# Performance work log

Measured on AMD Instinct MI355X. Metric: run time of the kernel, lower is better.

Reference implementation:

```python
import jax, jax.numpy as jnp
import numpy as np

B, S, D, H, NE, M = 4, 512, 768, 12, 42, 8
OFFSET = 1  # bert cls offset


def setup_inputs() -> dict:
    key = jax.random.key(0)
    k1, k2, k3, k4 = jax.random.split(key, 4)
    sequence_output = jax.random.normal(k1, (B, S, D), dtype=jnp.float32)
    attention = jax.random.uniform(k2, (B, H, S, S), dtype=jnp.float32)
    mention_pos = jax.random.randint(k3, (B, NE, M), 0, S - 2, dtype=jnp.int32)
    mention_mask = jax.random.randint(k4, (B, NE, M), 0, 2, dtype=jnp.int32)
    mention_mask = mention_mask.at[..., 0].set(1)  # every entity has >=1 mention
    return {"sequence_output": sequence_output, "attention": attention,
            "mention_pos": mention_pos, "mention_mask": mention_mask}


def reference(sequence_output, attention, mention_pos, mention_mask):
    b, s, d = sequence_output.shape
    h = attention.shape[1]
    pos = mention_pos + OFFSET                      # [B,NE,M]
    valid = (mention_mask > 0) & (pos < s)          # start+offset < c check
    pos_c = jnp.clip(pos, 0, s - 1)
    bidx = jnp.arange(b)[:, None, None]

    # ragged gather of mention hidden states / attention rows
    emb_m = sequence_output[bidx, pos_c]            # [B,NE,M,D]
    att_m = attention[bidx, :, pos_c]               # [B,NE,M,H,S]

    # logsumexp pool over valid mentions (zeros if no valid mention)
    masked = jnp.where(valid[..., None], emb_m, -jnp.inf)
    lse = jax.scipy.special.logsumexp(masked, axis=2)          # [B,NE,D]
    has = valid.any(axis=2)
    ent_emb = jnp.where(has[..., None], lse, 0.0)

    # mean pool attention rows over valid mentions
    cnt = jnp.maximum(valid.sum(axis=2), 1).astype(att_m.dtype)
    ent_att = (att_m * valid[..., None, None].astype(att_m.dtype)).sum(axis=2) \
              / cnt[..., None, None]                            # [B,NE,H,S]

    # all-pairs head/tail entity embeddings (index_select over hts pairs)
    hs = jnp.broadcast_to(ent_emb[:, :, None, :], (b, NE, NE, d))
    ts = jnp.broadcast_to(ent_emb[:, None, :, :], (b, NE, NE, d))

    # context-based channel map: pairwise attention fusion
    ht = (ent_att[:, :, None] * ent_att[:, None, :]).mean(axis=3)  # [B,NE,NE,S]
    ht = ht / (ht.sum(axis=-1, keepdims=True) + 1e-5)
    rs = jnp.einsum('bsd,bijs->bijd', sequence_output, ht)         # [B,NE,NE,D]

    return jnp.concatenate([hs, ts, rs], axis=-1)  # [B,NE,NE,3D]
```

## Files before the change

kernel.cpp:

```cpp
#include <hip/hip_runtime.h>
#include <hip/hip_bf16.h>
#include <cfloat>
#include <cmath>

#define B_ 4
#define S_ 512
#define D_ 768
#define H_ 12
#define NE_ 42
#define M_ 8
#define OFFSET_ 1
#define NE2_ (NE_*NE_)
#define OUTC_ (3*D_)
#define HS_ (H_*S_)
#define MPAD_ 1792

typedef __attribute__((ext_vector_type(8))) short short8;
typedef __attribute__((ext_vector_type(4))) float f32x4;

#define GLOAD_LDS16(g, l) __builtin_amdgcn_global_load_lds( \
    (const __attribute__((address_space(1))) unsigned int*)(g), \
    (__attribute__((address_space(3))) unsigned int*)(l), 16, 0, 0)

__global__ void k_prep(const float* __restrict__ seq, __hip_bfloat16* __restrict__ seqT) {
    const int b  = blockIdx.z;
    const int s0 = blockIdx.y * 64;
    const int d0 = blockIdx.x * 64;
    const int t  = threadIdx.x;

    __shared__ float tile[64][65];
#pragma unroll
    for (int i = 0; i < 16; ++i) {
        const int r = (t >> 6) * 16 + i;
        const int c = t & 63;
        tile[r][c] = seq[((size_t)b * S_ + s0 + r) * D_ + d0 + c];
    }
    __syncthreads();
#pragma unroll
    for (int i = 0; i < 16; ++i) {
        const int r = (t >> 6) * 16 + i;
        const int c = t & 63;
        seqT[((size_t)b * D_ + d0 + r) * S_ + s0 + c] = __float2bfloat16(tile[c][r]);
    }
}

__global__ void k_ent_att(const float* __restrict__ att, const int* __restrict__ mpos,
                          const int* __restrict__ mmask, float* __restrict__ ent_att) {
    const int beh = blockIdx.x;
    const int h   = beh % H_;
    const int be  = beh / H_;
    const int b   = be / NE_;

    __shared__ int sp[M_];
    __shared__ int sv[M_];
    if (threadIdx.x < M_) {
        int p  = mpos[be * M_ + threadIdx.x] + OFFSET_;
        int v  = (mmask[be * M_ + threadIdx.x] > 0) && (p < S_);
        int pc = p < 0 ? 0 : (p > S_ - 1 ? S_ - 1 : p);
        sp[threadIdx.x] = pc;
        sv[threadIdx.x] = v;
    }
    __syncthreads();

    int cnt = 0;
#pragma unroll
    for (int m = 0; m < M_; ++m) cnt += sv[m];
    const float inv_cnt = 1.0f / (float)(cnt > 0 ? cnt : 1);

    const float* arow = att + ((size_t)b * H_ + h) * S_ * S_;
    const int s0 = threadIdx.x;
    const int s1 = threadIdx.x + 256;
    float a0 = 0.0f, a1 = 0.0f;
#pragma unroll
    for (int m = 0; m < M_; ++m) {
        if (sv[m]) {
            a0 += arow[(size_t)sp[m] * S_ + s0];
            a1 += arow[(size_t)sp[m] * S_ + s1];
        }
    }
    float* dst = ent_att + ((size_t)be * H_ + h) * S_;
    dst[s0] = a0 * inv_cnt;
    dst[s1] = a1 * inv_cnt;
}

__global__ void k_ent_emb(const float* __restrict__ seq, const int* __restrict__ mpos,
                          const int* __restrict__ mmask, float* __restrict__ ent_emb) {
    const int be = blockIdx.x;
    const int b  = be / NE_;

    __shared__ int sp[M_];
    __shared__ int sv[M_];
    if (threadIdx.x < M_) {
        int p  = mpos[be * M_ + threadIdx.x] + OFFSET_;
        int v  = (mmask[be * M_ + threadIdx.x] > 0) && (p < S_);
        int pc = p < 0 ? 0 : (p > S_ - 1 ? S_ - 1 : p);
        sp[threadIdx.x] = pc;
        sv[threadIdx.x] = v;
    }
    __syncthreads();

    int cnt = 0;
#pragma unroll
    for (int m = 0; m < M_; ++m) cnt += sv[m];
    const bool has = cnt > 0;

    for (int d = threadIdx.x; d < D_; d += blockDim.x) {
        float vals[M_];
        float mx = -FLT_MAX;
#pragma unroll
        for (int m = 0; m < M_; ++m) {
            float v = sv[m] ? seq[((size_t)b * S_ + sp[m]) * D_ + d] : -FLT_MAX;
            vals[m] = v;
            mx = fmaxf(mx, v);
        }
        float o = 0.0f;
        if (has) {
            float ss = 0.0f;
#pragma unroll
            for (int m = 0; m < M_; ++m)
                if (sv[m]) ss += expf(vals[m] - mx);
            o = mx + logf(ss);
        }
        ent_emb[(size_t)be * D_ + d] = o;
    }
}

__global__ void k_ht(const float* __restrict__ ent_att, __hip_bfloat16* __restrict__ htb) {
    const int ij = blockIdx.x;
    const int b  = blockIdx.y;
    const int s0 = threadIdx.x;
    const int s1 = threadIdx.x + 256;
    __hip_bfloat16* dst = htb + ((size_t)b * MPAD_ + ij) * S_;

    if (ij >= NE2_) {
        dst[s0] = __float2bfloat16(0.0f);
        dst[s1] = __float2bfloat16(0.0f);
        return;
    }
    const int i = ij / NE_;
    const int j = ij - i * NE_;

    const float* Ai = ent_att + ((size_t)b * NE_ + i) * HS_;
    const float* Aj = ent_att + ((size_t)b * NE_ + j) * HS_;

    float v0 = 0.0f, v1 = 0.0f;
#pragma unroll
    for (int h = 0; h < H_; ++h) {
        v0 += Ai[h * S_ + s0] * Aj[h * S_ + s0];
        v1 += Ai[h * S_ + s1] * Aj[h * S_ + s1];
    }
    v0 *= (1.0f / H_);
    v1 *= (1.0f / H_);

    float local = v0 + v1;
#pragma unroll
    for (int off = 32; off > 0; off >>= 1) local += __shfl_xor(local, off, 64);
    __shared__ float wsum[4];
    if ((threadIdx.x & 63) == 0) wsum[threadIdx.x >> 6] = local;
    __syncthreads();
    const float inv = 1.0f / (wsum[0] + wsum[1] + wsum[2] + wsum[3] + 1e-5f);

    dst[s0] = __float2bfloat16(v0 * inv);
    dst[s1] = __float2bfloat16(v1 * inv);
}

__global__ void __launch_bounds__(256)
k_gemm(const __hip_bfloat16* __restrict__ htb, const __hip_bfloat16* __restrict__ seqT,
       float* __restrict__ out) {
    const int b     = blockIdx.z;
    const int tileN = blockIdx.x * 128;
    const int tileM = blockIdx.y * 128;
    const int tid   = threadIdx.x;
    const int w     = tid >> 6;
    const int lane  = tid & 63;
    const int wr    = w >> 1;
    const int wc    = w & 1;

    __shared__ unsigned short As[128 * 32];
    __shared__ unsigned short Bs[128 * 32];

    const __hip_bfloat16* A = htb  + (size_t)b * MPAD_ * S_;
    const __hip_bfloat16* Bt = seqT + (size_t)b * D_ * S_;

    const int crow = lane >> 2;
    const int ccol = (lane & 3) * 8;

    const int lr = lane & 15;
    const int lk = (lane >> 4) * 8;

    f32x4 acc[4][4];
#pragma unroll
    for (int mf = 0; mf < 4; ++mf)
#pragma unroll
        for (int nf = 0; nf < 4; ++nf) acc[mf][nf] = (f32x4){0.f, 0.f, 0.f, 0.f};

    for (int k0 = 0; k0 < S_; k0 += 32) {
#pragma unroll
        for (int q = 0; q < 2; ++q) {
            const int c = w * 2 + q;
            const __hip_bfloat16* ga = A + (size_t)(tileM + c * 16 + crow) * S_ + k0 + ccol;
            GLOAD_LDS16(ga, As + c * 512);
            const __hip_bfloat16* gb = Bt + (size_t)(tileN + c * 16 + crow) * S_ + k0 + ccol;
            GLOAD_LDS16(gb, Bs + c * 512);
        }
        __syncthreads();

        short8 af[4], bf[4];
#pragma unroll
        for (int mf = 0; mf < 4; ++mf)
            af[mf] = *(const short8*)&As[(wr * 64 + mf * 16 + lr) * 32 + lk];
#pragma unroll
        for (int nf = 0; nf < 4; ++nf)
            bf[nf] = *(const short8*)&Bs[(wc * 64 + nf * 16 + lr) * 32 + lk];
#pragma unroll
        for (int mf = 0; mf < 4; ++mf)
#pragma unroll
            for (int nf = 0; nf < 4; ++nf)
                acc[mf][nf] = __builtin_amdgcn_mfma_f32_16x16x32_bf16(af[mf], bf[nf], acc[mf][nf], 0, 0, 0);
        __syncthreads();
    }

#pragma unroll
    for (int mf = 0; mf < 4; ++mf) {
        const int row0 = tileM + wr * 64 + mf * 16 + (lane >> 4) * 4;
#pragma unroll
        for (int nf = 0; nf < 4; ++nf) {
            const int col = tileN + wc * 64 + nf * 16 + (lane & 15);
#pragma unroll
            for (int j = 0; j < 4; ++j) {
                const int r = row0 + j;
                if (r < NE2_)
                    out[((size_t)(b * NE2_ + r)) * OUTC_ + 2 * D_ + col] = acc[mf][nf][j];
            }
        }
    }
}

__global__ void k_hsts(const float* __restrict__ ent_emb, float* __restrict__ out) {
    const int bij = blockIdx.x;
    const int b   = bij / NE2_;
    const int ij  = bij - b * NE2_;
    const int i   = ij / NE_;
    const int j   = ij - i * NE_;

    const float4* ei = reinterpret_cast<const float4*>(ent_emb + ((size_t)b * NE_ + i) * D_);
    const float4* ej = reinterpret_cast<const float4*>(ent_emb + ((size_t)b * NE_ + j) * D_);
    float4* o = reinterpret_cast<float4*>(out + (size_t)bij * OUTC_);

    for (int t = threadIdx.x; t < D_ / 4; t += blockDim.x) o[t] = ei[t];
    for (int t = threadIdx.x; t < D_ / 4; t += blockDim.x) o[D_ / 4 + t] = ej[t];
}

extern "C" void kernel_launch(void* const* d_in, const int* in_sizes, int n_in,
                              void* d_out, int out_size, void* d_ws, size_t ws_size,
                              hipStream_t stream) {
    const float* seq   = (const float*)d_in[0];
    const float* att   = (const float*)d_in[1];
    const int*   mpos  = (const int*)d_in[2];
    const int*   mmask = (const int*)d_in[3];
    float* out = (float*)d_out;

    float* ent_emb = (float*)d_ws;
    float* ent_att = ent_emb + (size_t)B_ * NE_ * D_;
    __hip_bfloat16* htb  = (__hip_bfloat16*)(ent_att + (size_t)B_ * NE_ * HS_);
    __hip_bfloat16* seqT = htb + (size_t)B_ * MPAD_ * S_;

    k_prep<<<dim3(D_ / 64, S_ / 64, B_), 256, 0, stream>>>(seq, seqT);
    k_ent_att<<<B_ * NE_ * H_, 256, 0, stream>>>(att, mpos, mmask, ent_att);
    k_ent_emb<<<B_ * NE_, 256, 0, stream>>>(seq, mpos, mmask, ent_emb);
    k_ht<<<dim3(MPAD_, B_), 256, 0, stream>>>(ent_att, htb);
    k_gemm<<<dim3(D_ / 128, MPAD_ / 128, B_), 256, 0, stream>>>(htb, seqT, out);
    k_hsts<<<B_ * NE2_, 256, 0, stream>>>(ent_emb, out);
}
```

Baseline: 149.9 us.

## Register-tile pairwise attention products and fold normalization into GEMM epilogue

Replaces the per-pair ht kernel with a kernel that stages an 8-column slice of every entity's attention in LDS. Each thread computes a 3x3 block of entity pairs, so each attention value is reused across many pairs instead of being re-read from global memory for every pair. The row-sum normalization is deferred: per-pair partial sums are accumulated into a zero-initialized buffer with atomics, and the GEMM epilogue scales each output row by the reciprocal, with the 1/H factor folded into the epsilon. This cuts redundant L2 traffic, at the cost of global atomics, an extra scalar load per output element in the epilogue, and padding rows of the A matrix that are no longer zeroed.

```diff
diff --git a/kernel.cpp b/kernel.cpp
--- a/kernel.cpp
+++ b/kernel.cpp
@@ -45,7 +45,16 @@
 }
 
 __global__ void k_ent_att(const float* __restrict__ att, const int* __restrict__ mpos,
-                          const int* __restrict__ mmask, float* __restrict__ ent_att) {
+                          const int* __restrict__ mmask, float* __restrict__ ent_att,
+                          float* __restrict__ Gsum) {
+    if (blockIdx.x < 7) {
+#pragma unroll
+        for (int k = 0; k < 4; ++k) {
+            const int idx = blockIdx.x * 1024 + k * 256 + threadIdx.x;
+            if (idx < B_ * NE2_) Gsum[idx] = 0.0f;
+        }
+    }
+
     const int beh = blockIdx.x;
     const int h   = beh % H_;
     const int be  = beh / H_;
@@ -125,48 +134,87 @@
     }
 }
 
-__global__ void k_ht(const float* __restrict__ ent_att, __hip_bfloat16* __restrict__ htb) {
-    const int ij = blockIdx.x;
-    const int b  = blockIdx.y;
-    const int s0 = threadIdx.x;
-    const int s1 = threadIdx.x + 256;
-    __hip_bfloat16* dst = htb + ((size_t)b * MPAD_ + ij) * S_;
-
-    if (ij >= NE2_) {
-        dst[s0] = __float2bfloat16(0.0f);
-        dst[s1] = __float2bfloat16(0.0f);
-        return;
-    }
-    const int i = ij / NE_;
-    const int j = ij - i * NE_;
-
-    const float* Ai = ent_att + ((size_t)b * NE_ + i) * HS_;
-    const float* Aj = ent_att + ((size_t)b * NE_ + j) * HS_;
-
-    float v0 = 0.0f, v1 = 0.0f;
-#pragma unroll
-    for (int h = 0; h < H_; ++h) {
-        v0 += Ai[h * S_ + s0] * Aj[h * S_ + s0];
-        v1 += Ai[h * S_ + s1] * Aj[h * S_ + s1];
-    }
-    v0 *= (1.0f / H_);
-    v1 *= (1.0f / H_);
-
-    float local = v0 + v1;
-#pragma unroll
-    for (int off = 32; off > 0; off >>= 1) local += __shfl_xor(local, off, 64);
-    __shared__ float wsum[4];
-    if ((threadIdx.x & 63) == 0) wsum[threadIdx.x >> 6] = local;
+__global__ void k_ht_raw(const float* __restrict__ ent_att,
+                         __hip_bfloat16* __restrict__ raw,
+                         float* __restrict__ Gsum) {
+    const int sc0 = blockIdx.x * 8;
+    const int b   = blockIdx.y;
+    const int t   = threadIdx.x;
+
+    __shared__ float lds[NE_ * 100];
+
+#pragma unroll
+    for (int k = 0; k < 4; ++k) {
+        const int q = t + k * 256;
+        if (q < 1008) {
+            const int e   = q / 24;
+            const int rem = q - e * 24;
+            const int h   = rem >> 1;
+            const int s4  = (rem & 1) * 4;
+            const float4 v = *reinterpret_cast<const float4*>(
+                &ent_att[(((size_t)b * NE_ + e) * H_ + h) * S_ + sc0 + s4]);
+            *reinterpret_cast<float4*>(&lds[e * 100 + h * 8 + s4]) = v;
+        }
+    }
     __syncthreads();
-    const float inv = 1.0f / (wsum[0] + wsum[1] + wsum[2] + wsum[3] + 1e-5f);
-
-    dst[s0] = __float2bfloat16(v0 * inv);
-    dst[s1] = __float2bfloat16(v1 * inv);
+
+    if (t >= 196) return;
+    const int ti = t / 14;
+    const int tj = t - ti * 14;
+    const int i0 = ti * 3, j0 = tj * 3;
+
+    float acc[3][3][8];
+#pragma unroll
+    for (int di = 0; di < 3; ++di)
+#pragma unroll
+        for (int dj = 0; dj < 3; ++dj)
+#pragma unroll
+            for (int v = 0; v < 8; ++v) acc[di][dj][v] = 0.0f;
+
+#pragma unroll
+    for (int s4 = 0; s4 < 2; ++s4) {
+#pragma unroll
+        for (int h = 0; h < H_; ++h) {
+            float4 ai[3], aj[3];
+#pragma unroll
+            for (int di = 0; di < 3; ++di)
+                ai[di] = *reinterpret_cast<const float4*>(&lds[(i0 + di) * 100 + h * 8 + s4 * 4]);
+#pragma unroll
+            for (int dj = 0; dj < 3; ++dj)
+                aj[dj] = *reinterpret_cast<const float4*>(&lds[(j0 + dj) * 100 + h * 8 + s4 * 4]);
+#pragma unroll
+            for (int di = 0; di < 3; ++di)
+#pragma unroll
+                for (int dj = 0; dj < 3; ++dj) {
+#pragma unroll
+                    for (int v = 0; v < 4; ++v)
+                        acc[di][dj][s4 * 4 + v] = fmaf(ai[di][v], aj[dj][v], acc[di][dj][s4 * 4 + v]);
+                }
+        }
+    }
+
+#pragma unroll
+    for (int di = 0; di < 3; ++di) {
+#pragma unroll
+        for (int dj = 0; dj < 3; ++dj) {
+            const int pair = (i0 + di) * NE_ + (j0 + dj);
+            __hip_bfloat16 tmp[8];
+            float g = 0.0f;
+#pragma unroll
+            for (int v = 0; v < 8; ++v) {
+                g += acc[di][dj][v];
+                tmp[v] = __float2bfloat16(acc[di][dj][v]);
+            }
+            *reinterpret_cast<short8*>(&raw[((size_t)b * MPAD_ + pair) * S_ + sc0]) =
+                *reinterpret_cast<short8*>(tmp);
+            atomicAdd(&Gsum[b * NE2_ + pair], g);
+        }
+    }
 }
 
 __global__ void __launch_bounds__(256)
 k_gemm(const __hip_bfloat16* __restrict__ htb, const __hip_bfloat16* __restrict__ seqT,
-       float* __restrict__ out) {
+       const float* __restrict__ Gsum, float* __restrict__ out) {
     const int b     = blockIdx.z;
     const int tileN = blockIdx.x * 128;
     const int tileM = blockIdx.y * 128;
@@ -229,8 +277,11 @@
 #pragma unroll
             for (int j = 0; j < 4; ++j) {
                 const int r = row0 + j;
-                if (r < NE2_)
-                    out[((size_t)(b * NE2_ + r)) * OUTC_ + 2 * D_ + col] = acc[mf][nf][j];
+                if (r < NE2_) {
+                    const float g  = Gsum[b * NE2_ + r];
+                    const float sc = 1.0f / (g + (float)H_ * 1e-5f);
+                    out[((size_t)(b * NE2_ + r)) * OUTC_ + 2 * D_ + col] = acc[mf][nf][j] * sc;
+                }
             }
         }
     }
@@ -262,13 +313,14 @@
 
     float* ent_emb = (float*)d_ws;
     float* ent_att = ent_emb + (size_t)B_ * NE_ * D_;
-    __hip_bfloat16* htb  = (__hip_bfloat16*)(ent_att + (size_t)B_ * NE_ * HS_);
-    __hip_bfloat16* seqT = htb + (size_t)B_ * MPAD_ * S_;
+    float* Gsum    = ent_att + (size_t)B_ * NE_ * HS_;
+    __hip_bfloat16* htraw = (__hip_bfloat16*)(Gsum + (size_t)B_ * NE2_);
+    __hip_bfloat16* seqT  = htraw + (size_t)B_ * MPAD_ * S_;
 
     k_prep<<<dim3(D_ / 64, S_ / 64, B_), 256, 0, stream>>>(seq, seqT);
-    k_ent_att<<<B_ * NE_ * H_, 256, 0, stream>>>(att, mpos, mmask, ent_att);
+    k_ent_att<<<B_ * NE_ * H_, 256, 0, stream>>>(att, mpos, mmask, ent_att, Gsum);
     k_ent_emb<<<B_ * NE_, 256, 0, stream>>>(seq, mpos, mmask, ent_emb);
-    k_ht<<<dim3(MPAD_, B_), 256, 0, stream>>>(ent_att, htb);
-    k_gemm<<<dim3(D_ / 128, MPAD_ / 128, B_), 256, 0, stream>>>(htb, seqT, out);
+    k_ht_raw<<<dim3(S_ / 8, B_), 256, 0, stream>>>(ent_att, htraw, Gsum);
+    k_gemm<<<dim3(D_ / 128, MPAD_ / 128, B_), 256, 0, stream>>>(htraw, seqT, Gsum, out);
     k_hsts<<<B_ * NE2_, 256, 0, stream>>>(ent_emb, out);
 }
```

Result: slower. 191.0 us (+27.4%).

## Double-buffer GEMM LDS tiles, halve N tile, vectorize k_ht loads/stores

Applied to the files above, without the earlier changes.

The GEMM now double-buffers its LDS tiles, issuing the next K-slice's global-to-LDS loads before computing on the current slice, with one barrier per iteration. The N tile shrinks from 128 to 64, which doubles the grid from 336 to 672 blocks to fill more CUs. k_ht switches to float2 loads and bf16x2 stores, with each thread handling two adjacent columns. The costs are more LDS per block, lower per-block arithmetic intensity, and more redundant A-tile reads across the extra N blocks.

```diff
diff --git a/kernel.cpp b/kernel.cpp
--- a/kernel.cpp
+++ b/kernel.cpp
@@ -128,13 +128,14 @@
 __global__ void k_ht(const float* __restrict__ ent_att, __hip_bfloat16* __restrict__ htb) {
     const int ij = blockIdx.x;
     const int b  = blockIdx.y;
-    const int s0 = threadIdx.x;
-    const int s1 = threadIdx.x + 256;
+    const int t  = threadIdx.x;
     __hip_bfloat16* dst = htb + ((size_t)b * MPAD_ + ij) * S_;
 
     if (ij >= NE2_) {
-        dst[s0] = __float2bfloat16(0.0f);
-        dst[s1] = __float2bfloat16(0.0f);
+        __hip_bfloat162 z;
+        z.x = __float2bfloat16(0.0f);
+        z.y = __float2bfloat16(0.0f);
+        *reinterpret_cast<__hip_bfloat162*>(&dst[2 * t]) = z;
         return;
     }
     const int i = ij / NE_;
@@ -146,8 +147,10 @@
     float v0 = 0.0f, v1 = 0.0f;
 #pragma unroll
     for (int h = 0; h < H_; ++h) {
-        v0 += Ai[h * S_ + s0] * Aj[h * S_ + s0];
-        v1 += Ai[h * S_ + s1] * Aj[h * S_ + s1];
+        const float2 a = *reinterpret_cast<const float2*>(&Ai[h * S_ + 2 * t]);
+        const float2 c = *reinterpret_cast<const float2*>(&Aj[h * S_ + 2 * t]);
+        v0 = fmaf(a.x, c.x, v0);
+        v1 = fmaf(a.y, c.y, v1);
     }
     v0 *= (1.0f / H_);
     v1 *= (1.0f / H_);
@@ -156,19 +159,21 @@
 #pragma unroll
     for (int off = 32; off > 0; off >>= 1) local += __shfl_xor(local, off, 64);
     __shared__ float wsum[4];
-    if ((threadIdx.x & 63) == 0) wsum[threadIdx.x >> 6] = local;
+    if ((t & 63) == 0) wsum[t >> 6] = local;
     __syncthreads();
     const float inv = 1.0f / (wsum[0] + wsum[1] + wsum[2] + wsum[3] + 1e-5f);
 
-    dst[s0] = __float2bfloat16(v0 * inv);
-    dst[s1] = __float2bfloat16(v1 * inv);
+    __hip_bfloat162 r;
+    r.x = __float2bfloat16(v0 * inv);
+    r.y = __float2bfloat16(v1 * inv);
+    *reinterpret_cast<__hip_bfloat162*>(&dst[2 * t]) = r;
 }
 
 __global__ void __launch_bounds__(256)
 k_gemm(const __hip_bfloat16* __restrict__ htb, const __hip_bfloat16* __restrict__ seqT,
        float* __restrict__ out) {
     const int b     = blockIdx.z;
-    const int tileN = blockIdx.x * 128;
+    const int tileN = blockIdx.x * 64;
     const int tileM = blockIdx.y * 128;
     const int tid   = threadIdx.x;
     const int w     = tid >> 6;
@@ -176,10 +181,10 @@
     const int wr    = w >> 1;
     const int wc    = w & 1;
 
-    __shared__ unsigned short As[128 * 32];
-    __shared__ unsigned short Bs[128 * 32];
-
-    const __hip_bfloat16* A = htb  + (size_t)b * MPAD_ * S_;
+    __shared__ unsigned short As[2][128 * 32];
+    __shared__ unsigned short Bs[2][64 * 32];
+
+    const __hip_bfloat16* A  = htb  + (size_t)b * MPAD_ * S_;
     const __hip_bfloat16* Bt = seqT + (size_t)b * D_ * S_;
 
     const int crow = lane >> 2;
@@ -188,35 +193,49 @@
     const int lr = lane & 15;
     const int lk = (lane >> 4) * 8;
 
-    f32x4 acc[4][4];
+    f32x4 acc[4][2];
 #pragma unroll
     for (int mf = 0; mf < 4; ++mf)
 #pragma unroll
-        for (int nf = 0; nf < 4; ++nf) acc[mf][nf] = (f32x4){0.f, 0.f, 0.f, 0.f};
-
-    for (int k0 = 0; k0 < S_; k0 += 32) {
+        for (int nf = 0; nf < 2; ++nf) acc[mf][nf] = (f32x4){0.f, 0.f, 0.f, 0.f};
+
+    {
 #pragma unroll
         for (int q = 0; q < 2; ++q) {
             const int c = w * 2 + q;
-            const __hip_bfloat16* ga = A + (size_t)(tileM + c * 16 + crow) * S_ + k0 + ccol;
-            GLOAD_LDS16(ga, As + c * 512);
-            const __hip_bfloat16* gb = Bt + (size_t)(tileN + c * 16 + crow) * S_ + k0 + ccol;
-            GLOAD_LDS16(gb, Bs + c * 512);
-        }
-        __syncthreads();
-
-        short8 af[4], bf[4];
+            GLOAD_LDS16(A + (size_t)(tileM + c * 16 + crow) * S_ + ccol, &As[0][c * 512]);
+        }
+        GLOAD_LDS16(Bt + (size_t)(tileN + w * 16 + crow) * S_ + ccol, &Bs[0][w * 512]);
+    }
+    __syncthreads();
+
+    for (int it = 0; it < 16; ++it) {
+        const int cur = it & 1;
+        if (it < 15) {
+            const int k0 = (it + 1) * 32;
+#pragma unroll
+            for (int q = 0; q < 2; ++q) {
+                const int c = w * 2 + q;
+                GLOAD_LDS16(A + (size_t)(tileM + c * 16 + crow) * S_ + k0 + ccol,
+                            &As[cur ^ 1][c * 512]);
+            }
+            GLOAD_LDS16(Bt + (size_t)(tileN + w * 16 + crow) * S_ + k0 + ccol,
+                        &Bs[cur ^ 1][w * 512]);
+        }
+
+        short8 af[4], bfr[2];
 #pragma unroll
         for (int mf = 0; mf < 4; ++mf)
-            af[mf] = *(const short8*)&As[(wr * 64 + mf * 16 + lr) * 32 + lk];
-#pragma unroll
-        for (int nf = 0; nf < 4; ++nf)
-            bf[nf] = *(const short8*)&Bs[(wc * 64 + nf * 16 + lr) * 32 + lk];
+            af[mf] = *(const short8*)&As[cur][(wr * 64 + mf * 16 + lr) * 32 + lk];
+#pragma unroll
+        for (int nf = 0; nf < 2; ++nf)
+            bfr[nf] = *(const short8*)&Bs[cur][(wc * 32 + nf * 16 + lr) * 32 + lk];
 #pragma unroll
         for (int mf = 0; mf < 4; ++mf)
 #pragma unroll
-            for (int nf = 0; nf < 4; ++nf)
-                acc[mf][nf] = __builtin_amdgcn_mfma_f32_16x16x32_bf16(af[mf], bf[nf], acc[mf][nf], 0, 0, 0);
+            for (int nf = 0; nf < 2; ++nf)
+                acc[mf][nf] = __builtin_amdgcn_mfma_f32_16x16x32_bf16(af[mf], bfr[nf], acc[mf][nf], 0, 0, 0);
+
         __syncthreads();
     }
 
@@ -224,8 +243,8 @@
     for (int mf = 0; mf < 4; ++mf) {
         const int row0 = tileM + wr * 64 + mf * 16 + (lane >> 4) * 4;
 #pragma unroll
-        for (int nf = 0; nf < 4; ++nf) {
-            const int col = tileN + wc * 64 + nf * 16 + (lane & 15);
+        for (int nf = 0; nf < 2; ++nf) {
+            const int col = tileN + wc * 32 + nf * 16 + (lane & 15);
 #pragma unroll
             for (int j = 0; j < 4; ++j) {
                 const int r = row0 + j;
@@ -269,6 +288,6 @@
     k_ent_att<<<B_ * NE_ * H_, 256, 0, stream>>>(att, mpos, mmask, ent_att);
     k_ent_emb<<<B_ * NE_, 256, 0, stream>>>(seq, mpos, mmask, ent_emb);
     k_ht<<<dim3(MPAD_, B_), 256, 0, stream>>>(ent_att, htb);
-    k_gemm<<<dim3(D_ / 128, MPAD_ / 128, B_), 256, 0, stream>>>(htb, seqT, out);
+    k_gemm<<<dim3(D_ / 64, MPAD_ / 128, B_), 256, 0, stream>>>(htb, seqT, out);
     k_hsts<<<B_ * NE2_, 256, 0, stream>>>(ent_emb, out);
 }
```

New measurement: 157.0 us. 1.05x slower.
